# Optimization experiments

Hardware: AMD Instinct MI355X
Metric: run time of the kernel (lower is better)

The kernel has to match this reference:

```python
import jax, jax.numpy as jnp
import numpy as np


def setup_inputs() -> dict:
    key = jax.random.key(0)
    ks = jax.random.split(key, 9)
    B, S, D, E, I = 4, 2048, 1024, 8, 2048
    sd = 1.0 / np.sqrt(D)
    si = 1.0 / np.sqrt(I)
    return {
        "hidden_states": jax.random.normal(ks[0], (B, S, D), dtype=jnp.float32),
        "gate_w": jax.random.normal(ks[1], (D, E), dtype=jnp.float32) * sd,
        "expert_gate_w": jax.random.normal(ks[2], (E, D, I), dtype=jnp.float32) * sd,
        "expert_up_w": jax.random.normal(ks[3], (E, D, I), dtype=jnp.float32) * sd,
        "expert_down_w": jax.random.normal(ks[4], (E, I, D), dtype=jnp.float32) * si,
        "shared_gate_proj_w": jax.random.normal(ks[5], (D, I), dtype=jnp.float32) * sd,
        "shared_up_w": jax.random.normal(ks[6], (D, I), dtype=jnp.float32) * sd,
        "shared_down_w": jax.random.normal(ks[7], (I, D), dtype=jnp.float32) * si,
        "shared_expert_gate_w": jax.random.normal(ks[8], (D, 1), dtype=jnp.float32) * sd,
        "top_k": 2,
    }


def reference(hidden_states, gate_w, expert_gate_w, expert_up_w, expert_down_w,
              shared_gate_proj_w, shared_up_w, shared_down_w, shared_expert_gate_w,
              top_k):
    B, S, D = hidden_states.shape
    E = gate_w.shape[1]
    x = hidden_states.reshape(-1, D)            # [T, D]
    T = x.shape[0]

    # Router: softmax in fp32, top-k, dense per-token per-expert combine weights.
    gate_vals = x @ gate_w                      # [T, E]
    probs = jax.nn.softmax(gate_vals.astype(jnp.float32), axis=-1)
    top_w, top_i = jax.lax.top_k(probs, top_k)  # [T, K]
    dense_w = jnp.zeros((T, E), dtype=jnp.float32)
    dense_w = dense_w.at[jnp.arange(T)[:, None], top_i].set(top_w)
    dense_w = dense_w.astype(x.dtype)           # zero for unselected experts

    # All experts as batched SwiGLU GEMMs (tokens with zero weight contribute 0).
    g = jnp.einsum('td,edi->eti', x, expert_gate_w)
    u = jnp.einsum('td,edi->eti', x, expert_up_w)
    y = jnp.einsum('eti,eid->etd', jax.nn.silu(g) * u, expert_down_w)  # [E, T, D]
    moe_out = jnp.einsum('etd,te->td', y, dense_w)                      # [T, D]

    # Shared expert with sigmoid gate.
    shared = (jax.nn.silu(x @ shared_gate_proj_w) * (x @ shared_up_w)) @ shared_down_w
    shared = jax.nn.sigmoid(x @ shared_expert_gate_w) * shared

    final = (moe_out + shared).reshape(B, S, D)
    return final, gate_vals
```

## Files before the change

### kernel.cpp

```cpp
#include <hip/hip_runtime.h>

typedef __bf16 bf16x8 __attribute__((ext_vector_type(8)));
typedef float f32x4 __attribute__((ext_vector_type(4)));
typedef float f4 __attribute__((ext_vector_type(4)));
typedef unsigned short us8 __attribute__((ext_vector_type(8)));
typedef unsigned short us4 __attribute__((ext_vector_type(4)));

#define T_TOK 8192
#define DDIM 1024
#define NEXP 8
#define IDIM 2048
#define NCH 1024
#define RROWS 17408
#define ROWS_TOT (T_TOK + RROWS)

__device__ __forceinline__ unsigned short f2bf(float f) {
    unsigned u = __float_as_uint(f);
    u += 0x7fffu + ((u >> 16) & 1u);
    return (unsigned short)(u >> 16);
}

#define GLDS(src, dst) __builtin_amdgcn_global_load_lds( \
    (const __attribute__((address_space(1))) void*)(src), \
    (__attribute__((address_space(3))) void*)(dst), 16, 0, 0)

__device__ __forceinline__ int offs_of(const int* __restrict__ cnt, int e) {
    int o = 0;
    for (int i = 0; i < e; i++) o += (cnt[i] + 127) & ~127;
    return o;
}

__global__ __launch_bounds__(256) void router_kernel(
    const float* __restrict__ x, const float* __restrict__ gate_w,
    const float* __restrict__ sgw, float* __restrict__ gate_out,
    float* __restrict__ wdense, float* __restrict__ sgout,
    unsigned short* __restrict__ xb)
{
    __shared__ float lgw[DDIM * NEXP];
    __shared__ float lsg[DDIM];
    int tid = threadIdx.x;
    for (int i = tid; i < (DDIM * NEXP) / 4; i += 256)
        ((f4*)lgw)[i] = ((const f4*)gate_w)[i];
    for (int i = tid; i < DDIM / 4; i += 256)
        ((f4*)lsg)[i] = ((const f4*)sgw)[i];
    __syncthreads();

    int wid = tid >> 6, l = tid & 63;
    int t = blockIdx.x * 4 + wid;

    float acc[NEXP];
#pragma unroll
    for (int e = 0; e < NEXP; e++) acc[e] = 0.f;
    float accs = 0.f;
    const float* xr = x + (size_t)t * DDIM;
    unsigned short* xbr = xb + (size_t)t * DDIM;
#pragma unroll
    for (int j = 0; j < 4; j++) {
        int d0 = j * 256 + l * 4;
        f4 xv = *(const f4*)(xr + d0);
        us4 xo;
#pragma unroll
        for (int c = 0; c < 4; c++) {
            float xd = xv[c];
            xo[c] = f2bf(xd);
            int d = d0 + c;
#pragma unroll
            for (int e = 0; e < NEXP; e++) acc[e] += xd * lgw[d * NEXP + e];
            accs += xd * lsg[d];
        }
        *(us4*)(xbr + d0) = xo;
    }
#pragma unroll
    for (int off = 32; off > 0; off >>= 1) {
#pragma unroll
        for (int e = 0; e < NEXP; e++) acc[e] += __shfl_xor(acc[e], off);
        accs += __shfl_xor(accs, off);
    }
    if (l == 0) {
        float m = acc[0];
        for (int e = 1; e < NEXP; e++) m = fmaxf(m, acc[e]);
        float p[NEXP], s = 0.f;
        for (int e = 0; e < NEXP; e++) { p[e] = __expf(acc[e] - m); s += p[e]; }
        float inv = 1.f / s;
        int i1 = 0; float b1 = p[0];
        for (int e = 1; e < NEXP; e++) if (p[e] > b1) { b1 = p[e]; i1 = e; }
        int i2 = -1; float b2 = -1.f;
        for (int e = 0; e < NEXP; e++) if (e != i1 && p[e] > b2) { b2 = p[e]; i2 = e; }
        for (int e = 0; e < NEXP; e++) {
            gate_out[(size_t)t * NEXP + e] = acc[e];
            float w = (e == i1) ? b1 * inv : (e == i2) ? b2 * inv : 0.f;
            wdense[(size_t)t * NEXP + e] = w;
        }
        sgout[t] = 1.f / (1.f + __expf(-accs));
    }
}

__global__ __launch_bounds__(256) void bucket_kernel(
    const float* __restrict__ wdense, int* __restrict__ list,
    float* __restrict__ wl, int* __restrict__ cnt,
    int* __restrict__ te, int* __restrict__ tp)
{
    int e = blockIdx.x;
    int tid = threadIdx.x, wid = tid >> 6, l = tid & 63;
    __shared__ int wsum[4];
    int base = 0;
    int* le = list + (size_t)e * T_TOK;
    float* we = wl + (size_t)e * T_TOK;
    for (int t0 = 0; t0 < T_TOK; t0 += 256) {
        int tok = t0 + tid;
        float w = wdense[(size_t)tok * NEXP + e];
        bool f = w > 0.f;
        unsigned long long m = __ballot(f);
        int lp = __popcll(m & ((1ull << l) - 1ull));
        if (l == 0) wsum[wid] = __popcll(m);
        __syncthreads();
        int woff = 0;
#pragma unroll
        for (int i = 0; i < 4; i++) if (i < wid) woff += wsum[i];
        int btot = wsum[0] + wsum[1] + wsum[2] + wsum[3];
        if (f) {
            int pos = base + woff + lp;
            le[pos] = tok; we[pos] = w;
            int slot = 0;
            for (int e2 = 0; e2 < e; e2++)
                slot += (wdense[(size_t)tok * NEXP + e2] > 0.f) ? 1 : 0;
            te[tok * 2 + slot] = e;
            tp[tok * 2 + slot] = pos;
        }
        base += btot;
        __syncthreads();
    }
    if (tid == 0) cnt[e] = base;
    int align = (base + 255) & ~255;
    for (int i = base + tid; i < align; i += 256) { le[i] = 0; we[i] = 0.f; }
}

__global__ __launch_bounds__(256) void wcvt_gu_kernel(
    const float* __restrict__ egw, const float* __restrict__ euw,
    const float* __restrict__ sgp, const float* __restrict__ sup,
    unsigned short* __restrict__ pool, int c0)
{
    int j = blockIdx.y;
    int e = j >> 1, s = j & 1;
    const float* src = (e < 8) ? ((s ? euw : egw) + (size_t)e * DDIM * IDIM)
                               : (s ? sup : sgp);
    unsigned short* dst = pool + (size_t)j * NCH * DDIM;
    int tpc = NCH / 64;
    int tci = blockIdx.x % tpc, tri = blockIdx.x / tpc;
    int r0 = tri * 64;
    int cl0 = tci * 64;
    int cg0 = c0 + cl0;

    __shared__ unsigned short lds[64][72];
    int t = threadIdx.x;
    int tr = t >> 4, tcc = (t & 15) * 4;
#pragma unroll
    for (int jj = 0; jj < 4; jj++) {
        int r = tr + jj * 16;
        f4 v = *(const f4*)(src + (size_t)(r0 + r) * IDIM + cg0 + tcc);
#pragma unroll
        for (int k = 0; k < 4; k++) lds[r][tcc + k] = f2bf(v[k]);
    }
    __syncthreads();
    int orow = t >> 2, ss = t & 3;
    us8 v0, v1;
#pragma unroll
    for (int i = 0; i < 8; i++) {
        v0[i] = lds[ss * 16 + i][orow];
        v1[i] = lds[ss * 16 + 8 + i][orow];
    }
    unsigned short* op = dst + (size_t)(cl0 + orow) * DDIM + r0 + ss * 16;
    *(us8*)op = v0; *(us8*)(op + 8) = v1;
}

__global__ __launch_bounds__(256) void wcvt_d_kernel(
    const float* __restrict__ edw, const float* __restrict__ sdw,
    unsigned short* __restrict__ pool)
{
    int j = blockIdx.y;
    const float* src = (j < 8) ? edw + (size_t)j * IDIM * DDIM : sdw;
    unsigned short* dst = pool + (size_t)j * DDIM * IDIM;
    int tpc = DDIM / 64;
    int tci = blockIdx.x % tpc, tri = blockIdx.x / tpc;
    int rg0 = tri * 64;
    int cg0 = tci * 64;

    __shared__ unsigned short lds[64][72];
    int t = threadIdx.x;
    int tr = t >> 4, tcc = (t & 15) * 4;
#pragma unroll
    for (int jj = 0; jj < 4; jj++) {
        int r = tr + jj * 16;
        f4 v = *(const f4*)(src + (size_t)(rg0 + r) * DDIM + cg0 + tcc);
#pragma unroll
        for (int k = 0; k < 4; k++) lds[r][tcc + k] = f2bf(v[k]);
    }
    __syncthreads();
    int orow = t >> 2, ss = t & 3;
    us8 v0, v1;
#pragma unroll
    for (int i = 0; i < 8; i++) {
        v0[i] = lds[ss * 16 + i][orow];
        v1[i] = lds[ss * 16 + 8 + i][orow];
    }
    unsigned short* op = dst + (size_t)(cg0 + orow) * IDIM + rg0 + ss * 16;
    *(us8*)op = v0; *(us8*)(op + 8) = v1;
}

__global__ __launch_bounds__(512, 1) void gemm_gateup8(
    const unsigned short* __restrict__ A, const unsigned short* __restrict__ pool,
    unsigned short* __restrict__ H, const int* __restrict__ listb,
    const int* __restrict__ cnt, int c0)
{
    int z = blockIdx.z;
    const unsigned short *Bg, *Bu; const int* lst; int count, rowb;
    if (z == 0) {
        Bg = pool + (size_t)16 * NCH * DDIM; Bu = pool + (size_t)17 * NCH * DDIM;
        lst = nullptr; count = T_TOK; rowb = 0;
    } else {
        int e = z - 1;
        Bg = pool + (size_t)(e * 2) * NCH * DDIM; Bu = pool + (size_t)(e * 2 + 1) * NCH * DDIM;
        lst = listb + (size_t)e * T_TOK; count = cnt[e]; rowb = T_TOK + offs_of(cnt, e);
    }
    int d = blockIdx.y * 8 + blockIdx.x;
    int mt = ((d >> 3) >> 3) * 8 + (d & 7);
    int nt = (d >> 3) & 7;
    int m0 = mt * 256, n0 = nt * 128;
    if (m0 >= count) return;
    int climit = (count + 127) & ~127;
    const int NT = DDIM / 64;

    __shared__ unsigned short lds[2][32768];

    int tid = threadIdx.x, wid = tid >> 6, l = tid & 63;
    int wm = wid >> 1, wn = wid & 1;
    int lr = l & 15, lkg = l >> 4;

    int sb = tid & 7, sr = tid >> 3;
    int sk = (sb ^ (sr & 7)) << 3;
    const unsigned short* pa[2][2];
#pragma unroll
    for (int h = 0; h < 2; h++)
#pragma unroll
        for (int j = 0; j < 2; j++) {
            int rr = m0 + h * 128 + j * 64 + sr;
            int ga = lst ? lst[rr] : rr;
            pa[h][j] = A + (size_t)ga * DDIM + sk;
        }
    const unsigned short* pbg = Bg + (size_t)(n0 + sr) * DDIM + sk;
    const unsigned short* pbu = Bu + (size_t)(n0 + sr) * DDIM + sk;

#define GU_ST_A(sbuf, h, t) { \
    GLDS(pa[h][0] + (t) * 64, (sbuf) + (h) * 8192 + tid * 8); \
    GLDS(pa[h][1] + (t) * 64, (sbuf) + (h) * 8192 + 4096 + tid * 8); }
#define GU_ST_BG(sbuf, t) { \
    GLDS(pbg + (t) * 64, (sbuf) + 16384 + tid * 8); \
    GLDS(pbg + (size_t)64 * DDIM + (t) * 64, (sbuf) + 16384 + 4096 + tid * 8); }
#define GU_ST_BU(sbuf, t) { \
    GLDS(pbu + (t) * 64, (sbuf) + 24576 + tid * 8); \
    GLDS(pbu + (size_t)64 * DDIM + (t) * 64, (sbuf) + 24576 + 4096 + tid * 8); }

    {
        unsigned short* s0 = &lds[0][0];
        GU_ST_A(s0, 0, 0); GU_ST_A(s0, 1, 0); GU_ST_BG(s0, 0); GU_ST_BU(s0, 0);
        unsigned short* s1 = &lds[1][0];
        GU_ST_A(s1, 0, 1); GU_ST_A(s1, 1, 1); GU_ST_BG(s1, 1); GU_ST_BU(s1, 1);
    }

    int xorc = (lr & 7) << 3;
    int kx0 = (lkg * 8) ^ xorc;
    int kx1 = (32 + lkg * 8) ^ xorc;
    int aoff[4], boff[4];
#pragma unroll
    for (int mf = 0; mf < 4; mf++) {
        int r = wm * 64 + mf * 16 + lr;
        aoff[mf] = (r >> 7) * 8192 + (r & 127) * 64;
    }
#pragma unroll
    for (int nf = 0; nf < 4; nf++)
        boff[nf] = 16384 + (wn * 64 + nf * 16 + lr) * 64;

    f32x4 zero = {0.f, 0.f, 0.f, 0.f};
    f32x4 accg[4][4], accu[4][4];
#pragma unroll
    for (int m = 0; m < 4; m++)
#pragma unroll
        for (int n = 0; n < 4; n++) { accg[m][n] = zero; accu[m][n] = zero; }

    bf16x8 a[2][2], bg[4][2], bu[4][2];

#pragma unroll 1
    for (int t = 0; t < NT; t++) {
        const unsigned short* cb = &lds[t & 1][0];
        unsigned short* sbuf = &lds[t & 1][0];
        bool stg = (t + 2 < NT);

        if (t == NT - 1) { asm volatile("s_waitcnt vmcnt(0)" ::: "memory"); }
        else             { asm volatile("s_waitcnt vmcnt(8)" ::: "memory"); }
        __builtin_amdgcn_s_barrier();
#pragma unroll
        for (int mf = 0; mf < 2; mf++) {
            a[mf][0] = *(const bf16x8*)(cb + aoff[mf] + kx0);
            a[mf][1] = *(const bf16x8*)(cb + aoff[mf] + kx1);
        }
#pragma unroll
        for (int nf = 0; nf < 2; nf++) {
            bg[nf][0] = *(const bf16x8*)(cb + boff[nf] + kx0);
            bg[nf][1] = *(const bf16x8*)(cb + boff[nf] + kx1);
            bu[nf][0] = *(const bf16x8*)(cb + boff[nf] + 8192 + kx0);
            bu[nf][1] = *(const bf16x8*)(cb + boff[nf] + 8192 + kx1);
        }
        __builtin_amdgcn_s_setprio(1);
#pragma unroll
        for (int kh = 0; kh < 2; kh++)
#pragma unroll
            for (int mf = 0; mf < 2; mf++)
#pragma unroll
                for (int nf = 0; nf < 2; nf++) {
                    accg[mf][nf] = __builtin_amdgcn_mfma_f32_16x16x32_bf16(a[mf][kh], bg[nf][kh], accg[mf][nf], 0, 0, 0);
                    accu[mf][nf] = __builtin_amdgcn_mfma_f32_16x16x32_bf16(a[mf][kh], bu[nf][kh], accu[mf][nf], 0, 0, 0);
                }
        __builtin_amdgcn_s_setprio(0);

        __builtin_amdgcn_s_barrier();
#pragma unroll
        for (int nf = 2; nf < 4; nf++) {
            bg[nf][0] = *(const bf16x8*)(cb + boff[nf] + kx0);
            bg[nf][1] = *(const bf16x8*)(cb + boff[nf] + kx1);
            bu[nf][0] = *(const bf16x8*)(cb + boff[nf] + 8192 + kx0);
            bu[nf][1] = *(const bf16x8*)(cb + boff[nf] + 8192 + kx1);
        }
        __builtin_amdgcn_s_setprio(1);
#pragma unroll
        for (int kh = 0; kh < 2; kh++)
#pragma unroll
            for (int mf = 0; mf < 2; mf++)
#pragma unroll
                for (int nf = 2; nf < 4; nf++) {
                    accg[mf][nf] = __builtin_amdgcn_mfma_f32_16x16x32_bf16(a[mf][kh], bg[nf][kh], accg[mf][nf], 0, 0, 0);
                    accu[mf][nf] = __builtin_amdgcn_mfma_f32_16x16x32_bf16(a[mf][kh], bu[nf][kh], accu[mf][nf], 0, 0, 0);
                }
        __builtin_amdgcn_s_setprio(0);

        __builtin_amdgcn_s_barrier();
#pragma unroll
        for (int mf = 0; mf < 2; mf++) {
            a[mf][0] = *(const bf16x8*)(cb + aoff[2 + mf] + kx0);
            a[mf][1] = *(const bf16x8*)(cb + aoff[2 + mf] + kx1);
        }
        if (stg) { GU_ST_BG(sbuf, t + 2); }
        __builtin_amdgcn_s_setprio(1);
#pragma unroll
        for (int kh = 0; kh < 2; kh++)
#pragma unroll
            for (int mf = 0; mf < 2; mf++)
#pragma unroll
                for (int nf = 0; nf < 2; nf++) {
                    accg[2 + mf][nf] = __builtin_amdgcn_mfma_f32_16x16x32_bf16(a[mf][kh], bg[nf][kh], accg[2 + mf][nf], 0, 0, 0);
                    accu[2 + mf][nf] = __builtin_amdgcn_mfma_f32_16x16x32_bf16(a[mf][kh], bu[nf][kh], accu[2 + mf][nf], 0, 0, 0);
                }
        __builtin_amdgcn_s_setprio(0);

        __builtin_amdgcn_s_barrier();
        if (stg) { GU_ST_BU(sbuf, t + 2); GU_ST_A(sbuf, 0, t + 2); GU_ST_A(sbuf, 1, t + 2); }
        __builtin_amdgcn_s_setprio(1);
#pragma unroll
        for (int kh = 0; kh < 2; kh++)
#pragma unroll
            for (int mf = 0; mf < 2; mf++)
#pragma unroll
                for (int nf = 2; nf < 4; nf++) {
                    accg[2 + mf][nf] = __builtin_amdgcn_mfma_f32_16x16x32_bf16(a[mf][kh], bg[nf][kh], accg[2 + mf][nf], 0, 0, 0);
                    accu[2 + mf][nf] = __builtin_amdgcn_mfma_f32_16x16x32_bf16(a[mf][kh], bu[nf][kh], accu[2 + mf][nf], 0, 0, 0);
                }
        __builtin_amdgcn_s_setprio(0);
    }

#pragma unroll
    for (int mf = 0; mf < 4; mf++) {
        int rbase = m0 + wm * 64 + mf * 16 + lkg * 4;
#pragma unroll
        for (int nf = 0; nf < 4; nf++) {
            int col = c0 + n0 + wn * 64 + nf * 16 + lr;
#pragma unroll
            for (int r = 0; r < 4; r++) {
                int rloc = rbase + r;
                if (rloc < climit) {
                    float g = accg[mf][nf][r], u = accu[mf][nf][r];
                    float hv = g * (1.f / (1.f + __expf(-g))) * u;
                    H[(size_t)(rowb + rloc) * IDIM + col] = f2bf(hv);
                }
            }
        }
    }
}

__global__ __launch_bounds__(512, 2) void gemm_down8(
    const unsigned short* __restrict__ H, const unsigned short* __restrict__ pool,
    unsigned short* __restrict__ Y,
    const float* __restrict__ wlb, const float* __restrict__ sgo,
    const int* __restrict__ cnt)
{
    int z = blockIdx.z;
    const unsigned short* B; const float* coef; int count, rowb;
    if (z == 0) {
        B = pool + (size_t)8 * DDIM * IDIM;
        coef = sgo; count = T_TOK; rowb = 0;
    } else {
        int e = z - 1;
        B = pool + (size_t)e * DDIM * IDIM;
        coef = wlb + (size_t)e * T_TOK;
        count = cnt[e]; rowb = T_TOK + offs_of(cnt, e);
    }
    int d = blockIdx.y * 4 + blockIdx.x;
    int mt = ((d >> 3) >> 2) * 8 + (d & 7);
    int nt = (d >> 3) & 3;
    int m0 = mt * 256, n0 = nt * 256;
    if (m0 >= count) return;
    int climit = (count + 127) & ~127;
    const int NT = IDIM / 64;

    __shared__ unsigned short lds[2][32768];

    int tid = threadIdx.x, wid = tid >> 6, l = tid & 63;
    int wm = wid >> 2, wn = wid & 3;
    int lr = l & 15, lkg = l >> 4;

    int sb = tid & 7, sr = tid >> 3;
    int sk = (sb ^ (sr & 7)) << 3;
    const unsigned short* pah = H + (size_t)(rowb + m0 + sr) * IDIM + sk;
    const unsigned short* pb  = B + (size_t)(n0 + sr) * IDIM + sk;

#define DN_ST_A(sbuf, h, t) { \
    GLDS(pah + (size_t)((h) * 128) * IDIM + (t) * 64, (sbuf) + (h) * 8192 + tid * 8); \
    GLDS(pah + (size_t)((h) * 128 + 64) * IDIM + (t) * 64, (sbuf) + (h) * 8192 + 4096 + tid * 8); }
#define DN_ST_B(sbuf, h, t) { \
    GLDS(pb + (size_t)((h) * 128) * IDIM + (t) * 64, (sbuf) + 16384 + (h) * 8192 + tid * 8); \
    GLDS(pb + (size_t)((h) * 128 + 64) * IDIM + (t) * 64, (sbuf) + 16384 + (h) * 8192 + 4096 + tid * 8); }

    {
        unsigned short* s0 = &lds[0][0];
        DN_ST_A(s0, 0, 0); DN_ST_A(s0, 1, 0); DN_ST_B(s0, 0, 0); DN_ST_B(s0, 1, 0);
        unsigned short* s1 = &lds[1][0];
        DN_ST_A(s1, 0, 1); DN_ST_A(s1, 1, 1); DN_ST_B(s1, 0, 1); DN_ST_B(s1, 1, 1);
    }

    int xorc = (lr & 7) << 3;
    int kx0 = (lkg * 8) ^ xorc;
    int kx1 = (32 + lkg * 8) ^ xorc;
    int aoff[8], boff[4];
#pragma unroll
    for (int mf = 0; mf < 8; mf++)
        aoff[mf] = wm * 8192 + (mf * 16 + lr) * 64;
#pragma unroll
    for (int nf = 0; nf < 4; nf++)
        boff[nf] = 16384 + (wn * 64 + nf * 16 + lr) * 64;

    f32x4 zero = {0.f, 0.f, 0.f, 0.f};
    f32x4 acc[8][4];
#pragma unroll
    for (int m = 0; m < 8; m++)
#pragma unroll
        for (int n = 0; n < 4; n++) acc[m][n] = zero;

    bf16x8 a[4][2], b[4][2];

#pragma unroll 1
    for (int t = 0; t < NT; t++) {
        const unsigned short* cb = &lds[t & 1][0];
        unsigned short* sbuf = &lds[t & 1][0];
        bool stg = (t + 2 < NT);

        if (t == NT - 1) { asm volatile("s_waitcnt vmcnt(0)" ::: "memory"); }
        else             { asm volatile("s_waitcnt vmcnt(8)" ::: "memory"); }
        __builtin_amdgcn_s_barrier();
#pragma unroll
        for (int mf = 0; mf < 4; mf++) {
            a[mf][0] = *(const bf16x8*)(cb + aoff[mf] + kx0);
            a[mf][1] = *(const bf16x8*)(cb + aoff[mf] + kx1);
        }
#pragma unroll
        for (int nf = 0; nf < 2; nf++) {
            b[nf][0] = *(const bf16x8*)(cb + boff[nf] + kx0);
            b[nf][1] = *(const bf16x8*)(cb + boff[nf] + kx1);
        }
        __builtin_amdgcn_s_setprio(1);
#pragma unroll
        for (int kh = 0; kh < 2; kh++)
#pragma unroll
            for (int mf = 0; mf < 4; mf++)
#pragma unroll
                for (int nf = 0; nf < 2; nf++)
                    acc[mf][nf] = __builtin_amdgcn_mfma_f32_16x16x32_bf16(a[mf][kh], b[nf][kh], acc[mf][nf], 0, 0, 0);
        __builtin_amdgcn_s_setprio(0);

        __builtin_amdgcn_s_barrier();
#pragma unroll
        for (int nf = 2; nf < 4; nf++) {
            b[nf][0] = *(const bf16x8*)(cb + boff[nf] + kx0);
            b[nf][1] = *(const bf16x8*)(cb + boff[nf] + kx1);
        }
        __builtin_amdgcn_s_setprio(1);
#pragma unroll
        for (int kh = 0; kh < 2; kh++)
#pragma unroll
            for (int mf = 0; mf < 4; mf++)
#pragma unroll
                for (int nf = 2; nf < 4; nf++)
                    acc[mf][nf] = __builtin_amdgcn_mfma_f32_16x16x32_bf16(a[mf][kh], b[nf][kh], acc[mf][nf], 0, 0, 0);
        __builtin_amdgcn_s_setprio(0);

        __builtin_amdgcn_s_barrier();
#pragma unroll
        for (int mf = 0; mf < 4; mf++) {
            a[mf][0] = *(const bf16x8*)(cb + aoff[4 + mf] + kx0);
            a[mf][1] = *(const bf16x8*)(cb + aoff[4 + mf] + kx1);
        }
        if (stg) { DN_ST_B(sbuf, 0, t + 2); }
        __builtin_amdgcn_s_setprio(1);
#pragma unroll
        for (int kh = 0; kh < 2; kh++)
#pragma unroll
            for (int mf = 0; mf < 4; mf++)
#pragma unroll
                for (int nf = 0; nf < 2; nf++)
                    acc[4 + mf][nf] = __builtin_amdgcn_mfma_f32_16x16x32_bf16(a[mf][kh], b[nf][kh], acc[4 + mf][nf], 0, 0, 0);
        __builtin_amdgcn_s_setprio(0);

        __builtin_amdgcn_s_barrier();
        if (stg) { DN_ST_B(sbuf, 1, t + 2); DN_ST_A(sbuf, 0, t + 2); DN_ST_A(sbuf, 1, t + 2); }
        __builtin_amdgcn_s_setprio(1);
#pragma unroll
        for (int kh = 0; kh < 2; kh++)
#pragma unroll
            for (int mf = 0; mf < 4; mf++)
#pragma unroll
                for (int nf = 2; nf < 4; nf++)
                    acc[4 + mf][nf] = __builtin_amdgcn_mfma_f32_16x16x32_bf16(a[mf][kh], b[nf][kh], acc[4 + mf][nf], 0, 0, 0);
        __builtin_amdgcn_s_setprio(0);
    }

#pragma unroll
    for (int mf = 0; mf < 8; mf++) {
        int rbase = m0 + wm * 128 + mf * 16 + lkg * 4;
        float cf[4];
#pragma unroll
        for (int r = 0; r < 4; r++) {
            int rloc = rbase + r;
            cf[r] = (rloc < climit) ? coef[rloc] : 0.f;
        }
#pragma unroll
        for (int nf = 0; nf < 4; nf++) {
            int col = n0 + wn * 64 + nf * 16 + lr;
#pragma unroll
            for (int r = 0; r < 4; r++) {
                int rloc = rbase + r;
                if (rloc < climit)
                    Y[(size_t)(rowb + rloc) * DDIM + col] = f2bf(cf[r] * acc[mf][nf][r]);
            }
        }
    }
}

__global__ __launch_bounds__(256) void combine_kernel(
    const unsigned short* __restrict__ Y, const int* __restrict__ te,
    const int* __restrict__ tp, const int* __restrict__ cnt,
    float* __restrict__ out)
{
    int off[NEXP];
    {
        int o = 0;
#pragma unroll
        for (int i = 0; i < NEXP; i++) { off[i] = o; o += (cnt[i] + 127) & ~127; }
    }
    int t = blockIdx.x * 2 + (threadIdx.x >> 7);
    int c = (threadIdx.x & 127) * 8;
    int e0 = te[2 * t], e1 = te[2 * t + 1];
    size_t r0 = (size_t)T_TOK + off[e0] + tp[2 * t];
    size_t r1 = (size_t)T_TOK + off[e1] + tp[2 * t + 1];

    us8 vs = *(const us8*)(Y + (size_t)t * DDIM + c);
    us8 v0 = *(const us8*)(Y + r0 * DDIM + c);
    us8 v1 = *(const us8*)(Y + r1 * DDIM + c);
    f4 o0, o1;
#pragma unroll
    for (int k = 0; k < 4; k++) {
        o0[k] = __uint_as_float((unsigned)vs[k] << 16)
              + __uint_as_float((unsigned)v0[k] << 16)
              + __uint_as_float((unsigned)v1[k] << 16);
        o1[k] = __uint_as_float((unsigned)vs[4 + k] << 16)
              + __uint_as_float((unsigned)v0[4 + k] << 16)
              + __uint_as_float((unsigned)v1[4 + k] << 16);
    }
    float* op = out + (size_t)t * DDIM + c;
    *(f4*)op = o0;
    *(f4*)(op + 4) = o1;
}

extern "C" void kernel_launch(void* const* d_in, const int* in_sizes, int n_in,
                              void* d_out, int out_size, void* d_ws, size_t ws_size,
                              hipStream_t stream)
{
    const float* x   = (const float*)d_in[0];
    const float* gw  = (const float*)d_in[1];
    const float* egw = (const float*)d_in[2];
    const float* euw = (const float*)d_in[3];
    const float* edw = (const float*)d_in[4];
    const float* sgp = (const float*)d_in[5];
    const float* sup = (const float*)d_in[6];
    const float* sdw = (const float*)d_in[7];
    const float* seg = (const float*)d_in[8];

    float* out0 = (float*)d_out;
    float* gate_out = out0 + (size_t)T_TOK * DDIM;

    char* ws = (char*)d_ws;
    auto take = [&](size_t bytes) { char* p = ws; ws += (bytes + 255) & ~(size_t)255; return p; };
    unsigned short* xb   = (unsigned short*)take((size_t)T_TOK * DDIM * 2);
    float* wdense = (float*)take((size_t)T_TOK * NEXP * 4);
    float* sgo    = (float*)take((size_t)T_TOK * 4);
    int*   list   = (int*)take((size_t)NEXP * T_TOK * 4);
    float* wl     = (float*)take((size_t)NEXP * T_TOK * 4);
    int*   cnt    = (int*)take(256);
    int*   offs_unused = (int*)take(256);
    int*   te     = (int*)take((size_t)T_TOK * 2 * 4);
    int*   tp     = (int*)take((size_t)T_TOK * 2 * 4);
    unsigned short* pool = (unsigned short*)take((size_t)18 * NCH * DDIM * 2);
    unsigned short* H    = (unsigned short*)take((size_t)ROWS_TOT * IDIM * 2);
    unsigned short* Y    = (unsigned short*)take((size_t)ROWS_TOT * DDIM * 2);
    (void)offs_unused;

    router_kernel<<<T_TOK / 4, 256, 0, stream>>>(x, gw, seg, gate_out, wdense, sgo, xb);
    bucket_kernel<<<NEXP, 256, 0, stream>>>(wdense, list, wl, cnt, te, tp);

    for (int c = 0; c < 2; c++) {
        int c0 = c * NCH;
        wcvt_gu_kernel<<<dim3((NCH / 64) * 16, 18), 256, 0, stream>>>(
            egw, euw, sgp, sup, pool, c0);
        gemm_gateup8<<<dim3(NCH / 128, T_TOK / 256, 9), 512, 0, stream>>>(
            xb, pool, H, list, cnt, c0);
    }

    wcvt_d_kernel<<<dim3((IDIM / 64) * 16, 9), 256, 0, stream>>>(edw, sdw, pool);
    gemm_down8<<<dim3(DDIM / 256, T_TOK / 256, 9), 512, 0, stream>>>(
        H, pool, Y, wl, sgo, cnt);

    combine_kernel<<<T_TOK / 2, 256, 0, stream>>>(Y, te, tp, cnt, out0);
}
```

Before: 548.8 us.

## Retile down-projection GEMM to 256x128 tiles with a 4x2 wave layout

Changes the down-projection GEMM's output tile from 256x256 to 256x128, arranges the eight waves as 4x2 with 64x64 per wave, halves the accumulator registers, and doubles the grid along N. The LDS stage drops to 48 KB per buffer. The intent is more blocks per expert, which gives better load balance and CU fill across the variable per-expert token counts. In exchange, arithmetic intensity per tile falls, H rows are re-read twice as often, and launch_bounds now declares one block per CU.

```diff
diff --git a/kernel.cpp b/kernel.cpp
--- a/kernel.cpp
+++ b/kernel.cpp
@@ -395,7 +395,7 @@
     }
 }
 
-__global__ __launch_bounds__(512, 2) void gemm_down8(
+__global__ __launch_bounds__(512, 1) void gemm_down8(
     const unsigned short* __restrict__ H, const unsigned short* __restrict__ pool,
     unsigned short* __restrict__ Y,
     const float* __restrict__ wlb, const float* __restrict__ sgo,
@@ -412,58 +412,63 @@
         coef = wlb + (size_t)e * T_TOK;
         count = cnt[e]; rowb = T_TOK + offs_of(cnt, e);
     }
-    int d = blockIdx.y * 4 + blockIdx.x;
-    int mt = ((d >> 3) >> 2) * 8 + (d & 7);
-    int nt = (d >> 3) & 3;
-    int m0 = mt * 256, n0 = nt * 256;
+    int d = blockIdx.y * 8 + blockIdx.x;
+    int mt = ((d >> 3) >> 3) * 8 + (d & 7);
+    int nt = (d >> 3) & 7;
+    int m0 = mt * 256, n0 = nt * 128;
     if (m0 >= count) return;
     int climit = (count + 127) & ~127;
     const int NT = IDIM / 64;
 
-    __shared__ unsigned short lds[2][32768];
+    __shared__ unsigned short lds[2][24576];
 
     int tid = threadIdx.x, wid = tid >> 6, l = tid & 63;
-    int wm = wid >> 2, wn = wid & 3;
+    int wm = wid >> 1, wn = wid & 1;
     int lr = l & 15, lkg = l >> 4;
 
     int sb = tid & 7, sr = tid >> 3;
     int sk = (sb ^ (sr & 7)) << 3;
-    const unsigned short* pah = H + (size_t)(rowb + m0 + sr) * IDIM + sk;
-    const unsigned short* pb  = B + (size_t)(n0 + sr) * IDIM + sk;
-
-#define DN_ST_A(sbuf, h, t) { \
-    GLDS(pah + (size_t)((h) * 128) * IDIM + (t) * 64, (sbuf) + (h) * 8192 + tid * 8); \
-    GLDS(pah + (size_t)((h) * 128 + 64) * IDIM + (t) * 64, (sbuf) + (h) * 8192 + 4096 + tid * 8); }
-#define DN_ST_B(sbuf, h, t) { \
-    GLDS(pb + (size_t)((h) * 128) * IDIM + (t) * 64, (sbuf) + 16384 + (h) * 8192 + tid * 8); \
-    GLDS(pb + (size_t)((h) * 128 + 64) * IDIM + (t) * 64, (sbuf) + 16384 + (h) * 8192 + 4096 + tid * 8); }
+    const unsigned short* pa[4];
+#pragma unroll
+    for (int h = 0; h < 4; h++)
+        pa[h] = H + (size_t)(rowb + m0 + h * 64 + sr) * IDIM + sk;
+    const unsigned short* pb = B + (size_t)(n0 + sr) * IDIM + sk;
+
+#define DNW_ST_A(sbuf, t) { \
+    GLDS(pa[0] + (t) * 64, (sbuf) + tid * 8); \
+    GLDS(pa[1] + (t) * 64, (sbuf) + 4096 + tid * 8); \
+    GLDS(pa[2] + (t) * 64, (sbuf) + 8192 + tid * 8); \
+    GLDS(pa[3] + (t) * 64, (sbuf) + 12288 + tid * 8); }
+#define DNW_ST_B(sbuf, t) { \
+    GLDS(pb + (t) * 64, (sbuf) + 16384 + tid * 8); \
+    GLDS(pb + (size_t)64 * IDIM + (t) * 64, (sbuf) + 16384 + 4096 + tid * 8); }
 
     {
         unsigned short* s0 = &lds[0][0];
-        DN_ST_A(s0, 0, 0); DN_ST_A(s0, 1, 0); DN_ST_B(s0, 0, 0); DN_ST_B(s0, 1, 0);
+        DNW_ST_A(s0, 0); DNW_ST_B(s0, 0);
         unsigned short* s1 = &lds[1][0];
-        DN_ST_A(s1, 0, 1); DN_ST_A(s1, 1, 1); DN_ST_B(s1, 0, 1); DN_ST_B(s1, 1, 1);
+        DNW_ST_A(s1, 1); DNW_ST_B(s1, 1);
     }
 
     int xorc = (lr & 7) << 3;
     int kx0 = (lkg * 8) ^ xorc;
     int kx1 = (32 + lkg * 8) ^ xorc;
-    int aoff[8], boff[4];
-#pragma unroll
-    for (int mf = 0; mf < 8; mf++)
-        aoff[mf] = wm * 8192 + (mf * 16 + lr) * 64;
+    int aoff[4], boff[4];
+#pragma unroll
+    for (int mf = 0; mf < 4; mf++)
+        aoff[mf] = (wm * 64 + mf * 16 + lr) * 64;
 #pragma unroll
     for (int nf = 0; nf < 4; nf++)
         boff[nf] = 16384 + (wn * 64 + nf * 16 + lr) * 64;
 
     f32x4 zero = {0.f, 0.f, 0.f, 0.f};
-    f32x4 acc[8][4];
-#pragma unroll
-    for (int m = 0; m < 8; m++)
+    f32x4 acc[4][4];
+#pragma unroll
+    for (int m = 0; m < 4; m++)
 #pragma unroll
         for (int n = 0; n < 4; n++) acc[m][n] = zero;
 
-    bf16x8 a[4][2], b[4][2];
+    bf16x8 a[2][2], b[4][2];
 
 #pragma unroll 1
     for (int t = 0; t < NT; t++) {
@@ -472,15 +477,15 @@
         bool stg = (t + 2 < NT);
 
         if (t == NT - 1) { asm volatile("s_waitcnt vmcnt(0)" ::: "memory"); }
-        else             { asm volatile("s_waitcnt vmcnt(8)" ::: "memory"); }
+        else             { asm volatile("s_waitcnt vmcnt(6)" ::: "memory"); }
         __builtin_amdgcn_s_barrier();
 #pragma unroll
-        for (int mf = 0; mf < 4; mf++) {
+        for (int mf = 0; mf < 2; mf++) {
             a[mf][0] = *(const bf16x8*)(cb + aoff[mf] + kx0);
             a[mf][1] = *(const bf16x8*)(cb + aoff[mf] + kx1);
         }
 #pragma unroll
-        for (int nf = 0; nf < 2; nf++) {
+        for (int nf = 0; nf < 4; nf++) {
             b[nf][0] = *(const bf16x8*)(cb + boff[nf] + kx0);
             b[nf][1] = *(const bf16x8*)(cb + boff[nf] + kx1);
         }
@@ -488,61 +493,45 @@
 #pragma unroll
         for (int kh = 0; kh < 2; kh++)
 #pragma unroll
-            for (int mf = 0; mf < 4; mf++)
-#pragma unroll
-                for (int nf = 0; nf < 2; nf++)
+            for (int mf = 0; mf < 2; mf++)
+#pragma unroll
+                for (int nf = 0; nf < 4; nf++)
                     acc[mf][nf] = __builtin_amdgcn_mfma_f32_16x16x32_bf16(a[mf][kh], b[nf][kh], acc[mf][nf], 0, 0, 0);
         __builtin_amdgcn_s_setprio(0);
 
         __builtin_amdgcn_s_barrier();
 #pragma unroll
-        for (int nf = 2; nf < 4; nf++) {
-            b[nf][0] = *(const bf16x8*)(cb + boff[nf] + kx0);
-            b[nf][1] = *(const bf16x8*)(cb + boff[nf] + kx1);
-        }
+        for (int mf = 0; mf < 2; mf++) {
+            a[mf][0] = *(const bf16x8*)(cb + aoff[2 + mf] + kx0);
+            a[mf][1] = *(const bf16x8*)(cb + aoff[2 + mf] + kx1);
+        }
+        if (stg) { DNW_ST_B(sbuf, t + 2); }
         __builtin_amdgcn_s_setprio(1);
 #pragma unroll
         for (int kh = 0; kh < 2; kh++)
 #pragma unroll
-            for (int mf = 0; mf < 4; mf++)
+            for (int mf = 0; mf < 2; mf++)
+#pragma unroll
+                for (int nf = 0; nf < 2; nf++)
+                    acc[2 + mf][nf] = __builtin_amdgcn_mfma_f32_16x16x32_bf16(a[mf][kh], b[nf][kh], acc[2 + mf][nf], 0, 0, 0);
+        __builtin_amdgcn_s_setprio(0);
+
+        __builtin_amdgcn_s_barrier();
+        if (stg) { DNW_ST_A(sbuf, t + 2); }
+        __builtin_amdgcn_s_setprio(1);
+#pragma unroll
+        for (int kh = 0; kh < 2; kh++)
+#pragma unroll
+            for (int mf = 0; mf < 2; mf++)
 #pragma unroll
                 for (int nf = 2; nf < 4; nf++)
-                    acc[mf][nf] = __builtin_amdgcn_mfma_f32_16x16x32_bf16(a[mf][kh], b[nf][kh], acc[mf][nf], 0, 0, 0);
+                    acc[2 + mf][nf] = __builtin_amdgcn_mfma_f32_16x16x32_bf16(a[mf][kh], b[nf][kh], acc[2 + mf][nf], 0, 0, 0);
         __builtin_amdgcn_s_setprio(0);
-
-        __builtin_amdgcn_s_barrier();
-#pragma unroll
-        for (int mf = 0; mf < 4; mf++) {
-            a[mf][0] = *(const bf16x8*)(cb + aoff[4 + mf] + kx0);
-            a[mf][1] = *(const bf16x8*)(cb + aoff[4 + mf] + kx1);
-        }
-        if (stg) { DN_ST_B(sbuf, 0, t + 2); }
-        __builtin_amdgcn_s_setprio(1);
-#pragma unroll
-        for (int kh = 0; kh < 2; kh++)
-#pragma unroll
-            for (int mf = 0; mf < 4; mf++)
-#pragma unroll
-                for (int nf = 0; nf < 2; nf++)
-                    acc[4 + mf][nf] = __builtin_amdgcn_mfma_f32_16x16x32_bf16(a[mf][kh], b[nf][kh], acc[4 + mf][nf], 0, 0, 0);
-        __builtin_amdgcn_s_setprio(0);
-
-        __builtin_amdgcn_s_barrier();
-        if (stg) { DN_ST_B(sbuf, 1, t + 2); DN_ST_A(sbuf, 0, t + 2); DN_ST_A(sbuf, 1, t + 2); }
-        __builtin_amdgcn_s_setprio(1);
-#pragma unroll
-        for (int kh = 0; kh < 2; kh++)
-#pragma unroll
-            for (int mf = 0; mf < 4; mf++)
-#pragma unroll
-                for (int nf = 2; nf < 4; nf++)
-                    acc[4 + mf][nf] = __builtin_amdgcn_mfma_f32_16x16x32_bf16(a[mf][kh], b[nf][kh], acc[4 + mf][nf], 0, 0, 0);
-        __builtin_amdgcn_s_setprio(0);
-    }
-
-#pragma unroll
-    for (int mf = 0; mf < 8; mf++) {
-        int rbase = m0 + wm * 128 + mf * 16 + lkg * 4;
+    }
+
+#pragma unroll
+    for (int mf = 0; mf < 4; mf++) {
+        int rbase = m0 + wm * 64 + mf * 16 + lkg * 4;
         float cf[4];
 #pragma unroll
         for (int r = 0; r < 4; r++) {
@@ -642,7 +631,7 @@
     }
 
     wcvt_d_kernel<<<dim3((IDIM / 64) * 16, 9), 256, 0, stream>>>(edw, sdw, pool);
-    gemm_down8<<<dim3(DDIM / 256, T_TOK / 256, 9), 512, 0, stream>>>(
+    gemm_down8<<<dim3(DDIM / 128, T_TOK / 256, 9), 512, 0, stream>>>(
         H, pool, Y, wl, sgo, cnt);
 
     combine_kernel<<<T_TOK / 2, 256, 0, stream>>>(Y, te, tp, cnt, out0);
```

Result: slower. 570.8 us (+4.0%).
